# Kernel optimization log

Hardware: AMD Instinct MI355X
Metric: run time of the kernel (lower is better)

The kernel has to match this reference:

```python
import jax, jax.numpy as jnp
import numpy as np

B, FEAT = 2048, 256
NUM_PIDS, CQ_SIZE = 30000, 8192
MOMENTUM = 0.5
SCALAR = 30.0
EPS_BN = 1e-5      # BatchNorm1d default eps
EPS_NORM = 1e-12   # F.normalize default eps


def l2norm(x):
    n = jnp.linalg.norm(x, axis=1, keepdims=True)
    return x / jnp.maximum(n, EPS_NORM)


def setup_inputs() -> dict:
    key = jax.random.key(0)
    k1, k2, k3, k4 = jax.random.split(key, 4)
    inputs = jax.random.normal(k1, (B, FEAT), jnp.float32)
    label = jax.random.randint(k2, (B,), 0, NUM_PIDS + 1)  # NUM_PIDS == ignore_index
    lut = jax.random.normal(k3, (NUM_PIDS, FEAT), jnp.float32)
    cq = jax.random.normal(k4, (CQ_SIZE, FEAT), jnp.float32)
    bn_weight = jnp.ones((FEAT,), jnp.float32)
    bn_bias = jnp.zeros((FEAT,), jnp.float32)
    return {"inputs": inputs, "label": label, "lut": lut, "cq": cq,
            "bn_weight": bn_weight, "bn_bias": bn_bias}


def reference(inputs, label, lut, cq, bn_weight, bn_bias):
    dtype = inputs.dtype
    rows = jnp.arange(B)

    # --- eval-mode BN on inputs (running stats at init: mean=0, var=1) ---
    norm_inputs = inputs / jnp.sqrt(jnp.asarray(1.0 + EPS_BN, dtype)) * bn_weight + bn_bias

    # --- bad-row masks (rows that are all zero) ---
    bad_lut_mask = jnp.all(lut == 0, axis=1)            # [P]
    good_lut = ~bad_lut_mask
    lc = jnp.minimum(label, NUM_PIDS - 1)
    bad_pos_mask = (label < NUM_PIDS) & bad_lut_mask[lc]  # label hits a bad lut row

    # --- train-mode masked BN over good lut rows (momentum=1.0 => running stats = batch stats) ---
    gm = good_lut[:, None].astype(dtype)
    n = jnp.sum(gm)
    mean = jnp.sum(lut * gm, axis=0) / n
    var = jnp.sum(((lut - mean) ** 2) * gm, axis=0) / n  # biased var for normalization
    lut_bn = jnp.where(good_lut[:, None],
                       (lut - mean) / jnp.sqrt(var + EPS_BN) * bn_weight + bn_bias,
                       lut)
    # running stats update happens under the hood (detached); unbiased var
    rm1 = jax.lax.stop_gradient(mean)
    rv1 = jax.lax.stop_gradient(var * n / (n - 1.0))

    qn = l2norm(norm_inputs)                              # [B, F]
    out_lab = qn @ l2norm(lut_bn).T                       # [B, P]
    out_lab = jnp.where(bad_lut_mask[None, :], jnp.asarray(-1.0, dtype), out_lab)
    out_lab = out_lab.at[rows, lc].set(
        jnp.where(bad_pos_mask, jnp.asarray(1.0, dtype), out_lab[rows, lc]))

    # --- eval-mode masked BN on cq using the just-updated running stats ---
    bad_cq_mask = jnp.all(cq == 0, axis=1)                # [Q]
    cq_bn = jnp.where(~bad_cq_mask[:, None],
                      (cq - rm1) / jnp.sqrt(rv1 + EPS_BN) * bn_weight + bn_bias,
                      cq)
    out_unl = qn @ l2norm(cq_bn).T                        # [B, Q]
    out_unl = jnp.where(bad_cq_mask[None, :], jnp.asarray(-1.0, dtype), out_unl)

    projected = jnp.concatenate([out_lab, out_unl], axis=1) * jnp.asarray(SCALAR, dtype)

    # --- cross entropy with ignore_index = NUM_PIDS, reduction='none', then sum/B ---
    logp = jax.nn.log_softmax(projected, axis=1)
    valid = label != NUM_PIDS
    per = -logp[rows, jnp.where(valid, label, 0)]
    per = jnp.where(valid, per, jnp.asarray(0.0, dtype))
    loss = jnp.sum(per) / B

    # --- serial momentum scatter into lut + circular-buffer enqueue into cq ---
    xs = jax.lax.stop_gradient(inputs)
    lut0 = jax.lax.stop_gradient(lut)
    cq0 = jax.lax.stop_gradient(cq)

    def step(carry, xy):
        lut_c, cq_c, hdr = carry
        x, y = xy
        is_lab = y < NUM_PIDS
        yc = jnp.minimum(y, NUM_PIDS - 1)
        new_row = jnp.where(is_lab, MOMENTUM * lut_c[yc] + (1.0 - MOMENTUM) * x, lut_c[yc])
        lut_c = lut_c.at[yc].set(new_row)
        cq_row = jnp.where(is_lab, cq_c[hdr], x)
        cq_c = cq_c.at[hdr].set(cq_row)
        hdr = jnp.where(is_lab, hdr, (hdr + 1) % CQ_SIZE)
        return (lut_c, cq_c, hdr), None

    (new_lut, new_cq, _), _ = jax.lax.scan(
        step, (lut0, cq0, jnp.asarray(0, label.dtype)), (xs, label))

    return loss, new_lut, new_cq
```

## Files before the change

kernel.cpp:

```cpp
#include <hip/hip_runtime.h>
#include <math.h>

#define NUM_PIDS 30000
#define CQ_SIZE  8192
#define BATCH    2048
#define FEAT     256
#define EPS_BN   1e-5f
#define EPS_NORM 1e-12f
#define SCALARV  30.0f

#define LUT_PAD  30080
#define NCOL     38272
#define BC       128
#define LUT_TILES 235
#define CT       299
#define RT       16
#define NWG      (CT*RT)
#define NB1      240
#define ROWS1    125
#define QPLANE   (BATCH*FEAT)

#define WS_Q1    0
#define WS_CB1   (WS_Q1 + BATCH*FEAT)
#define WS_CB2   (WS_CB1 + BATCH)
#define WS_RN2   (WS_CB2 + BATCH)
#define WS_FLAGS (WS_RN2 + 2*NCOL)
#define WS_PSUM  (WS_FLAGS + LUT_PAD)
#define WS_PSQ   (WS_PSUM + NB1*FEAT)
#define WS_PCNT  (WS_PSQ + NB1*FEAT)
#define WS_A1    (WS_PCNT + 256)
#define WS_B1    (WS_A1 + FEAT)
#define WS_A2    (WS_B1 + FEAT)
#define WS_B2    (WS_A2 + FEAT)
#define WS_ZT    (WS_B2 + FEAT)
#define WS_PART  (WS_ZT + BATCH)
#define WS_LOSS8 (WS_PART + BATCH*CT)
#define WS_XH    ((WS_LOSS8 + 8 + 3) & ~3)
#define WS_XL    (WS_XH + NCOL*FEAT/2)
#define WS_QP    (WS_XL + NCOL*FEAT/2)

typedef __bf16 bf16x8 __attribute__((ext_vector_type(8)));
typedef float  f32x4  __attribute__((ext_vector_type(4)));

__device__ __forceinline__ unsigned short f2bf(float f) {
  __bf16 h = (__bf16)f; return __builtin_bit_cast(unsigned short, h);
}
__device__ __forceinline__ float bf2f(unsigned short u) {
  __bf16 h = __builtin_bit_cast(__bf16, u); return (float)h;
}
__device__ __forceinline__ void gload_lds16(const void* g, void* l) {
  __builtin_amdgcn_global_load_lds((__attribute__((address_space(1))) void*)(g),
                                   (__attribute__((address_space(3))) void*)(l), 16, 0, 0);
}

__global__ __launch_bounds__(256) void k_stats1(const float* __restrict__ lut,
                                                float* __restrict__ ws,
                                                int* __restrict__ flags) {
  const int t = threadIdx.x;
  const int rbase = blockIdx.x * ROWS1;
  __shared__ unsigned char wz[ROWS1 * 4];
  float s = 0.f, sq = 0.f;
  for (int i = 0; i < ROWS1; ++i) {
    float v = lut[(size_t)(rbase + i) * FEAT + t];
    s += v; sq += v * v;
    unsigned long long bal = __ballot(v != 0.0f);
    if ((t & 63) == 0) wz[i * 4 + (t >> 6)] = (bal != 0ull) ? 1 : 0;
  }
  __syncthreads();
  for (int i = t; i < ROWS1; i += 256) {
    int bad = !(wz[i*4] | wz[i*4+1] | wz[i*4+2] | wz[i*4+3]);
    flags[rbase + i] = bad;
  }
  ws[WS_PSUM + blockIdx.x * FEAT + t] = s;
  ws[WS_PSQ  + blockIdx.x * FEAT + t] = sq;
  if (t == 0) {
    int cnt = 0;
    for (int i = 0; i < ROWS1; ++i)
      cnt += (wz[i*4] | wz[i*4+1] | wz[i*4+2] | wz[i*4+3]) ? 1 : 0;
    ws[WS_PCNT + blockIdx.x] = (float)cnt;
  }
}

__global__ __launch_bounds__(256) void k_stats2(const float* __restrict__ bnw,
                                                const float* __restrict__ bnb,
                                                float* __restrict__ ws) {
  const int t = threadIdx.x;
  float2* rn2 = (float2*)(ws + WS_RN2);
  float s = 0.f, sq = 0.f, n = 0.f;
  for (int b = 0; b < NB1; ++b) { s += ws[WS_PSUM + b*FEAT + t]; sq += ws[WS_PSQ + b*FEAT + t]; }
  for (int b = 0; b < NB1; ++b) n += ws[WS_PCNT + b];
  float mean = s / n;
  float var = fmaxf(sq / n - mean * mean, 0.f);
  float istd_b = rsqrtf(var + EPS_BN);
  float rv1 = var * n / (n - 1.f);
  float istd_u = rsqrtf(rv1 + EPS_BN);
  float w = bnw[t], b_ = bnb[t];
  float a1 = istd_b * w, a2 = istd_u * w;
  ws[WS_A1 + t] = a1; ws[WS_B1 + t] = b_ - mean * a1;
  ws[WS_A2 + t] = a2; ws[WS_B2 + t] = b_ - mean * a2;
  if (t < (LUT_PAD - NUM_PIDS)) rn2[NUM_PIDS + t] = make_float2(0.f, -1e30f);
}

__global__ __launch_bounds__(256) void k_prep(const float* __restrict__ lut,
                                              const float* __restrict__ cq,
                                              float* __restrict__ ws,
                                              unsigned short* __restrict__ xh,
                                              unsigned short* __restrict__ xl,
                                              float* __restrict__ out_lut,
                                              float* __restrict__ out_cq) {
  const int row = blockIdx.x * 4 + (threadIdx.x >> 6);
  const int ln = threadIdx.x & 63;
  float2* rn2 = (float2*)(ws + WS_RN2);
  if (row >= NUM_PIDS && row < LUT_PAD) {
    uint2 z = make_uint2(0u, 0u);
    *(uint2*)(xh + (size_t)row * FEAT + ln * 4) = z;
    *(uint2*)(xl + (size_t)row * FEAT + ln * 4) = z;
    return;
  }
  const float* src; const float* av; const float* bv; float* dst;
  if (row < NUM_PIDS) {
    src = lut + (size_t)row * FEAT; av = ws + WS_A1; bv = ws + WS_B1;
    dst = out_lut + (size_t)row * FEAT;
  } else {
    src = cq + (size_t)(row - LUT_PAD) * FEAT; av = ws + WS_A2; bv = ws + WS_B2;
    dst = out_cq + (size_t)(row - LUT_PAD) * FEAT;
  }
  float4 x = ((const float4*)src)[ln];
  float4 a = ((const float4*)av)[ln];
  float4 b = ((const float4*)bv)[ln];
  dst[ln*4+0] = x.x; dst[ln*4+1] = x.y; dst[ln*4+2] = x.z; dst[ln*4+3] = x.w;
  unsigned short h0 = f2bf(x.x), h1 = f2bf(x.y), h2 = f2bf(x.z), h3 = f2bf(x.w);
  unsigned short l0 = f2bf(x.x - bf2f(h0)), l1 = f2bf(x.y - bf2f(h1));
  unsigned short l2 = f2bf(x.z - bf2f(h2)), l3 = f2bf(x.w - bf2f(h3));
  *(uint2*)(xh + (size_t)row * FEAT + ln * 4) =
      make_uint2((unsigned)h0 | ((unsigned)h1 << 16), (unsigned)h2 | ((unsigned)h3 << 16));
  *(uint2*)(xl + (size_t)row * FEAT + ln * 4) =
      make_uint2((unsigned)l0 | ((unsigned)l1 << 16), (unsigned)l2 | ((unsigned)l3 << 16));
  bool nz = (x.x != 0.f) || (x.y != 0.f) || (x.z != 0.f) || (x.w != 0.f);
  unsigned long long bal = __ballot(nz);
  float t0 = a.x*x.x + b.x, t1 = a.y*x.y + b.y, t2 = a.z*x.z + b.z, t3 = a.w*x.w + b.w;
  float ssum = t0*t0 + t1*t1 + t2*t2 + t3*t3;
  for (int o = 32; o; o >>= 1) ssum += __shfl_xor(ssum, o);
  if (ln == 0) {
    rn2[row] = (bal == 0ull) ? make_float2(0.f, -SCALARV)
                             : make_float2(1.0f / fmaxf(sqrtf(ssum), EPS_NORM), 1e30f);
  }
}

__global__ __launch_bounds__(256) void k_qn(const float* __restrict__ inp,
                                            const float* __restrict__ bnw,
                                            const float* __restrict__ bnb,
                                            const int* __restrict__ label,
                                            const float* __restrict__ lut,
                                            float* __restrict__ ws,
                                            unsigned short* __restrict__ qp) {
  const int r = blockIdx.x, t = threadIdx.x;
  const float s0 = rsqrtf(1.0f + EPS_BN);
  float v = inp[(size_t)r * FEAT + t];
  float bn = v * (bnw[t] * s0) + bnb[t];
  float x = bn * bn;
  for (int o = 32; o; o >>= 1) x += __shfl_down(x, o);
  __shared__ float w4[4];
  __shared__ float w8[8];
  __shared__ float w4b[4];
  if ((t & 63) == 0) w4[t >> 6] = x;
  __syncthreads();
  float nsq = w4[0] + w4[1] + w4[2] + w4[3];
  float rinv = 1.0f / fmaxf(sqrtf(nsq), EPS_NORM);
  float qn = bn * rinv;
  float y1 = qn * ws[WS_B1 + t], y2 = qn * ws[WS_B2 + t];
  for (int o = 32; o; o >>= 1) { y1 += __shfl_down(y1, o); y2 += __shfl_down(y2, o); }
  if ((t & 63) == 0) { w8[t >> 6] = y1; w8[4 + (t >> 6)] = y2; }
  float q1 = qn * ws[WS_A1 + t], q2 = qn * ws[WS_A2 + t];
  size_t o1 = (size_t)r * FEAT + t;
  unsigned short h1 = f2bf(q1), h2 = f2bf(q2);
  qp[0*QPLANE + o1] = h1;
  qp[1*QPLANE + o1] = f2bf(q1 - bf2f(h1));
  qp[2*QPLANE + o1] = h2;
  qp[3*QPLANE + o1] = f2bf(q2 - bf2f(h2));
  __syncthreads();
  if (t == 0) {
    ws[WS_CB1 + r] = w8[0] + w8[1] + w8[2] + w8[3];
    ws[WS_CB2 + r] = w8[4] + w8[5] + w8[6] + w8[7];
  }
  const int* flags = (const int*)(ws + WS_FLAGS);
  const float2* rn2 = (const float2*)(ws + WS_RN2);
  int y = label[r];
  if (y >= NUM_PIDS) { if (t == 0) ws[WS_ZT + r] = 0.f; return; }
  if (flags[y] == 1) { if (t == 0) ws[WS_ZT + r] = SCALARV; return; }
  float xt = q1 * lut[(size_t)y * FEAT + t];
  for (int o = 32; o; o >>= 1) xt += __shfl_down(xt, o);
  if ((t & 63) == 0) w4b[t >> 6] = xt;
  __syncthreads();
  if (t == 0) {
    float dot = w4b[0] + w4b[1] + w4b[2] + w4b[3];
    float cb1 = w8[0] + w8[1] + w8[2] + w8[3];
    ws[WS_ZT + r] = SCALARV * rn2[y].x * (dot + cb1);
  }
}

__global__ __launch_bounds__(256) void k_gemm(const unsigned short* __restrict__ xh,
                                              const unsigned short* __restrict__ xl,
                                              const unsigned short* __restrict__ qp,
                                              float* __restrict__ ws) {
  __shared__ __align__(16) unsigned char smem[65536];
  const int tid = threadIdx.x;
  const int w = tid >> 6, l = tid & 63;
  const int bid = blockIdx.x;
  const int sid = (bid & 7) * (NWG / 8) + (bid >> 3);
  const int colT = sid >> 4, rowT = sid & 15;
  const bool islut = colT < LUT_TILES;
  const int colbase = colT * BC;
  const int rowbase = rowT * 128;

  const unsigned short* qh = qp + (islut ? 0 : 2) * QPLANE;
  const unsigned short* ql = qh + QPLANE;

  const int segc = l >> 3, slot = l & 7;
  const int kc8l = slot ^ segc;
  const unsigned short* gsrc;
  unsigned char* lbase;
  int gbase;
  if (w == 0)      { gsrc = xh; lbase = smem;         gbase = colbase; }
  else if (w == 1) { gsrc = xl; lbase = smem + 16384; gbase = colbase; }
  else if (w == 2) { gsrc = qh; lbase = smem + 32768; gbase = rowbase; }
  else             { gsrc = ql; lbase = smem + 49152; gbase = rowbase; }

  const int lc = l & 15, lk = l >> 4;
  const int wr = w >> 1, wc = w & 1;

  f32x4 acc[4][4];
#pragma unroll
  for (int rf = 0; rf < 4; ++rf)
#pragma unroll
    for (int cf = 0; cf < 4; ++cf) { f32x4 z = {0.f,0.f,0.f,0.f}; acc[rf][cf] = z; }

  for (int kc = 0; kc < 4; ++kc) {
    const int kb = kc * 64;
#pragma unroll
    for (int i = 0; i < 16; ++i) {
      const unsigned short* g = gsrc + (size_t)(gbase + i * 8 + segc) * FEAT + kb + kc8l * 8;
      gload_lds16(g, lbase + i * 1024);
    }
    __syncthreads();
#pragma unroll
    for (int ks = 0; ks < 2; ++ks) {
      const int kc8 = ks * 4 + lk;
      const int sA = (kc8 ^ (lc & 7)) * 16;
      bf16x8 ah[4], al[4], bh[4], bl[4];
#pragma unroll
      for (int rf = 0; rf < 4; ++rf) {
        int off = (wr * 64 + rf * 16 + lc) * 128 + sA;
        ah[rf] = *(const bf16x8*)(smem + 32768 + off);
        al[rf] = *(const bf16x8*)(smem + 49152 + off);
      }
#pragma unroll
      for (int cf = 0; cf < 4; ++cf) {
        int off = (wc * 64 + cf * 16 + lc) * 128 + sA;
        bh[cf] = *(const bf16x8*)(smem + off);
        bl[cf] = *(const bf16x8*)(smem + 16384 + off);
      }
#pragma unroll
      for (int rf = 0; rf < 4; ++rf)
#pragma unroll
        for (int cf = 0; cf < 4; ++cf) {
          acc[rf][cf] = __builtin_amdgcn_mfma_f32_16x16x32_bf16(ah[rf], bh[cf], acc[rf][cf], 0, 0, 0);
          acc[rf][cf] = __builtin_amdgcn_mfma_f32_16x16x32_bf16(ah[rf], bl[cf], acc[rf][cf], 0, 0, 0);
          acc[rf][cf] = __builtin_amdgcn_mfma_f32_16x16x32_bf16(al[rf], bh[cf], acc[rf][cf], 0, 0, 0);
        }
    }
    __syncthreads();
  }

  const float* cb = ws + (islut ? WS_CB1 : WS_CB2);
  const float2* rn2 = (const float2*)(ws + WS_RN2);
  float* red = (float*)smem;
#pragma unroll
  for (int rf = 0; rf < 4; ++rf) {
    float cbv[4];
#pragma unroll
    for (int r4 = 0; r4 < 4; ++r4)
      cbv[r4] = cb[rowbase + wr * 64 + rf * 16 + lk * 4 + r4];
    float part[4] = {0.f, 0.f, 0.f, 0.f};
#pragma unroll
    for (int cf = 0; cf < 4; ++cf) {
      float2 rc = rn2[colbase + wc * 64 + cf * 16 + lc];
#pragma unroll
      for (int r4 = 0; r4 < 4; ++r4) {
        float z = SCALARV * rc.x * (acc[rf][cf][r4] + cbv[r4]);
        z = fminf(z, rc.y);
        part[r4] += __expf(z - SCALARV);
      }
    }
#pragma unroll
    for (int r4 = 0; r4 < 4; ++r4) {
#pragma unroll
      for (int o = 1; o < 16; o <<= 1) part[r4] += __shfl_xor(part[r4], o);
      if (lc == 0) red[(wr * 64 + rf * 16 + lk * 4 + r4) * 2 + wc] = part[r4];
    }
  }
  __syncthreads();
  if (tid < 128) {
    float val = red[tid * 2] + red[tid * 2 + 1];
    ws[WS_PART + (size_t)colT * BATCH + rowbase + tid] = val;
  }
}

__global__ __launch_bounds__(256) void k_loss(const int* __restrict__ label,
                                              float* __restrict__ ws) {
  const int t = threadIdx.x;
  const int r = blockIdx.x * 256 + t;
  const int* flags = (const int*)(ws + WS_FLAGS);
  float ls = 0.f;
  int y = label[r];
  if (y < NUM_PIDS) {
    float ss = 0.f;
    const float* p = ws + WS_PART;
    for (int c = 0; c < CT; ++c) ss += p[(size_t)c * BATCH + r];
    if (flags[y] == 1) ss += 1.0f - __expf(-2.0f * SCALARV);
    ls = (SCALARV + __logf(ss)) - ws[WS_ZT + r];
  }
  for (int o = 32; o; o >>= 1) ls += __shfl_down(ls, o);
  __shared__ float w4[4];
  if ((t & 63) == 0) w4[t >> 6] = ls;
  __syncthreads();
  if (t == 0) ws[WS_LOSS8 + blockIdx.x] = w4[0] + w4[1] + w4[2] + w4[3];
}

__global__ void k_loss2(float* __restrict__ ws, float* __restrict__ out) {
  if (threadIdx.x == 0) {
    float s = 0.f;
    for (int i = 0; i < 8; ++i) s += ws[WS_LOSS8 + i];
    out[0] = s / (float)BATCH;
  }
}

__global__ __launch_bounds__(256) void k_lutcq(const int* __restrict__ label,
                                               const float* __restrict__ inp,
                                               const float* __restrict__ lut,
                                               float* __restrict__ out_lut,
                                               float* __restrict__ out_cq) {
  const int r = blockIdx.x, t = threadIdx.x;
  const int y = label[r];
  __shared__ unsigned long long mask[32];
  const int wv = t >> 6, ln = t & 63;
  const int wr_ = r >> 6, br_ = r & 63;
  if (y < NUM_PIDS) {
#pragma unroll
    for (int it = 0; it < 8; ++it) {
      int i = it * 256 + wv * 64 + ln;
      unsigned long long bal = __ballot(label[i] == y);
      if (ln == 0) mask[it * 4 + wv] = bal;
    }
    __syncthreads();
    unsigned long long selfbit = 1ull << br_;
    bool after = (mask[wr_] & ~((selfbit - 1) | selfbit)) != 0ull;
    for (int w2 = wr_ + 1; w2 < 32; ++w2) after = after || (mask[w2] != 0ull);
    if (after) return;
    float f = lut[(size_t)y * FEAT + t];
    for (int w2 = 0; w2 <= wr_; ++w2) {
      unsigned long long m = mask[w2];
      if (w2 == wr_) m &= (selfbit - 1) | selfbit;
      while (m) {
        int b = __ffsll((unsigned long long)m) - 1;
        m &= m - 1;
        int rr = w2 * 64 + b;
        f = 0.5f * f + 0.5f * inp[(size_t)rr * FEAT + t];
      }
    }
    out_lut[(size_t)y * FEAT + t] = f;
  } else {
#pragma unroll
    for (int it = 0; it < 8; ++it) {
      int i = it * 256 + wv * 64 + ln;
      unsigned long long bal = __ballot(label[i] == NUM_PIDS);
      if (ln == 0) mask[it * 4 + wv] = bal;
    }
    __syncthreads();
    int rank = 0;
    for (int w2 = 0; w2 < wr_; ++w2) rank += __popcll(mask[w2]);
    rank += __popcll(mask[wr_] & ((1ull << br_) - 1ull));
    out_cq[(size_t)rank * FEAT + t] = inp[(size_t)r * FEAT + t];
  }
}

extern "C" void kernel_launch(void* const* d_in, const int* in_sizes, int n_in,
                              void* d_out, int out_size, void* d_ws, size_t ws_size,
                              hipStream_t stream) {
  const float* inp = (const float*)d_in[0];
  const int* label = (const int*)d_in[1];
  const float* lut = (const float*)d_in[2];
  const float* cq  = (const float*)d_in[3];
  const float* bnw = (const float*)d_in[4];
  const float* bnb = (const float*)d_in[5];
  float* out = (float*)d_out;
  float* ws  = (float*)d_ws;
  int* flags = (int*)(ws + WS_FLAGS);
  unsigned short* xh = (unsigned short*)(ws + WS_XH);
  unsigned short* xl = (unsigned short*)(ws + WS_XL);
  unsigned short* qp = (unsigned short*)(ws + WS_QP);

  float* out_lut = out + 1;
  float* out_cq  = out + 1 + (size_t)NUM_PIDS * FEAT;

  k_stats1<<<NB1, 256, 0, stream>>>(lut, ws, flags);
  k_stats2<<<1, 256, 0, stream>>>(bnw, bnb, ws);
  k_prep<<<NCOL / 4, 256, 0, stream>>>(lut, cq, ws, xh, xl, out_lut, out_cq);
  k_qn<<<BATCH, 256, 0, stream>>>(inp, bnw, bnb, label, lut, ws, qp);
  k_lutcq<<<BATCH, 256, 0, stream>>>(label, inp, lut, out_lut, out_cq);
  k_gemm<<<NWG, 256, 0, stream>>>(xh, xl, qp, ws);
  k_loss<<<8, 256, 0, stream>>>(label, ws);
  k_loss2<<<1, 64, 0, stream>>>(ws, out);
}
```

Before: 347.4 us.

## Switch GEMM to 32x32 MFMA tiles and parallelize LUT stats reductions

```diff
diff --git a/kernel.cpp b/kernel.cpp
--- a/kernel.cpp
+++ b/kernel.cpp
@@ -16,8 +16,8 @@
 #define CT       299
 #define RT       16
 #define NWG      (CT*RT)
-#define NB1      240
-#define ROWS1    125
+#define NB1      600
+#define ROWS1    50
 #define QPLANE   (BATCH*FEAT)
 
 #define WS_Q1    0
@@ -28,7 +28,7 @@
 #define WS_PSUM  (WS_FLAGS + LUT_PAD)
 #define WS_PSQ   (WS_PSUM + NB1*FEAT)
 #define WS_PCNT  (WS_PSQ + NB1*FEAT)
-#define WS_A1    (WS_PCNT + 256)
+#define WS_A1    (WS_PCNT + 640)
 #define WS_B1    (WS_A1 + FEAT)
 #define WS_A2    (WS_B1 + FEAT)
 #define WS_B2    (WS_A2 + FEAT)
@@ -40,7 +40,7 @@
 #define WS_QP    (WS_XL + NCOL*FEAT/2)
 
 typedef __bf16 bf16x8 __attribute__((ext_vector_type(8)));
-typedef float  f32x4  __attribute__((ext_vector_type(4)));
+typedef float  f32x16 __attribute__((ext_vector_type(16)));
 
 __device__ __forceinline__ unsigned short f2bf(float f) {
   __bf16 h = (__bf16)f; return __builtin_bit_cast(unsigned short, h);
@@ -84,21 +84,35 @@
 __global__ __launch_bounds__(256) void k_stats2(const float* __restrict__ bnw,
                                                 const float* __restrict__ bnb,
                                                 float* __restrict__ ws) {
-  const int t = threadIdx.x;
+  const int fl = threadIdx.x & 31;
+  const int p  = threadIdx.x >> 5;
+  const int f  = blockIdx.x * 32 + fl;
   float2* rn2 = (float2*)(ws + WS_RN2);
+  __shared__ float ps[8][32], pq[8][32], pn[8];
   float s = 0.f, sq = 0.f, n = 0.f;
-  for (int b = 0; b < NB1; ++b) { s += ws[WS_PSUM + b*FEAT + t]; sq += ws[WS_PSQ + b*FEAT + t]; }
-  for (int b = 0; b < NB1; ++b) n += ws[WS_PCNT + b];
-  float mean = s / n;
-  float var = fmaxf(sq / n - mean * mean, 0.f);
-  float istd_b = rsqrtf(var + EPS_BN);
-  float rv1 = var * n / (n - 1.f);
-  float istd_u = rsqrtf(rv1 + EPS_BN);
-  float w = bnw[t], b_ = bnb[t];
-  float a1 = istd_b * w, a2 = istd_u * w;
-  ws[WS_A1 + t] = a1; ws[WS_B1 + t] = b_ - mean * a1;
-  ws[WS_A2 + t] = a2; ws[WS_B2 + t] = b_ - mean * a2;
-  if (t < (LUT_PAD - NUM_PIDS)) rn2[NUM_PIDS + t] = make_float2(0.f, -1e30f);
+  for (int b = p; b < NB1; b += 8) {
+    s  += ws[WS_PSUM + b * FEAT + f];
+    sq += ws[WS_PSQ  + b * FEAT + f];
+    n  += ws[WS_PCNT + b];
+  }
+  ps[p][fl] = s; pq[p][fl] = sq;
+  if (fl == 0) pn[p] = n;
+  __syncthreads();
+  if (p == 0) {
+    float S = 0.f, SQ = 0.f, N = 0.f;
+    for (int i = 0; i < 8; ++i) { S += ps[i][fl]; SQ += pq[i][fl]; N += pn[i]; }
+    float mean = S / N;
+    float var = fmaxf(SQ / N - mean * mean, 0.f);
+    float istd_b = rsqrtf(var + EPS_BN);
+    float rv1 = var * N / (N - 1.f);
+    float istd_u = rsqrtf(rv1 + EPS_BN);
+    float w = bnw[f], b_ = bnb[f];
+    float a1 = istd_b * w, a2 = istd_u * w;
+    ws[WS_A1 + f] = a1; ws[WS_B1 + f] = b_ - mean * a1;
+    ws[WS_A2 + f] = a2; ws[WS_B2 + f] = b_ - mean * a2;
+  }
+  if (blockIdx.x == 0 && threadIdx.x < (LUT_PAD - NUM_PIDS))
+    rn2[NUM_PIDS + threadIdx.x] = make_float2(0.f, -1e30f);
 }
 
 __global__ __launch_bounds__(256) void k_prep(const float* __restrict__ lut,
@@ -226,14 +240,14 @@
   else if (w == 2) { gsrc = qh; lbase = smem + 32768; gbase = rowbase; }
   else             { gsrc = ql; lbase = smem + 49152; gbase = rowbase; }
 
-  const int lc = l & 15, lk = l >> 4;
   const int wr = w >> 1, wc = w & 1;
-
-  f32x4 acc[4][4];
-#pragma unroll
-  for (int rf = 0; rf < 4; ++rf)
-#pragma unroll
-    for (int cf = 0; cf < 4; ++cf) { f32x4 z = {0.f,0.f,0.f,0.f}; acc[rf][cf] = z; }
+  const int l31 = l & 31, lhi = l >> 5;
+
+  f32x16 acc[2][2];
+#pragma unroll
+  for (int af = 0; af < 2; ++af)
+#pragma unroll
+    for (int cf = 0; cf < 2; ++cf) acc[af][cf] = (f32x16)(0.f);
 
   for (int kc = 0; kc < 4; ++kc) {
     const int kb = kc * 64;
@@ -244,29 +258,29 @@
     }
     __syncthreads();
 #pragma unroll
-    for (int ks = 0; ks < 2; ++ks) {
-      const int kc8 = ks * 4 + lk;
-      const int sA = (kc8 ^ (lc & 7)) * 16;
-      bf16x8 ah[4], al[4], bh[4], bl[4];
-#pragma unroll
-      for (int rf = 0; rf < 4; ++rf) {
-        int off = (wr * 64 + rf * 16 + lc) * 128 + sA;
-        ah[rf] = *(const bf16x8*)(smem + 32768 + off);
-        al[rf] = *(const bf16x8*)(smem + 49152 + off);
+    for (int kt = 0; kt < 4; ++kt) {
+      const int kc8 = kt * 2 + lhi;
+      const int sA = (kc8 ^ (l & 7)) * 16;
+      bf16x8 ah[2], al[2], bh[2], bl[2];
+#pragma unroll
+      for (int af = 0; af < 2; ++af) {
+        int off = (wr * 64 + af * 32 + l31) * 128 + sA;
+        ah[af] = *(const bf16x8*)(smem + 32768 + off);
+        al[af] = *(const bf16x8*)(smem + 49152 + off);
       }
 #pragma unroll
-      for (int cf = 0; cf < 4; ++cf) {
-        int off = (wc * 64 + cf * 16 + lc) * 128 + sA;
+      for (int cf = 0; cf < 2; ++cf) {
+        int off = (wc * 64 + cf * 32 + l31) * 128 + sA;
         bh[cf] = *(const bf16x8*)(smem + off);
         bl[cf] = *(const bf16x8*)(smem + 16384 + off);
       }
 #pragma unroll
-      for (int rf = 0; rf < 4; ++rf)
-#pragma unroll
-        for (int cf = 0; cf < 4; ++cf) {
-          acc[rf][cf] = __builtin_amdgcn_mfma_f32_16x16x32_bf16(ah[rf], bh[cf], acc[rf][cf], 0, 0, 0);
-          acc[rf][cf] = __builtin_amdgcn_mfma_f32_16x16x32_bf16(ah[rf], bl[cf], acc[rf][cf], 0, 0, 0);
-          acc[rf][cf] = __builtin_amdgcn_mfma_f32_16x16x32_bf16(al[rf], bh[cf], acc[rf][cf], 0, 0, 0);
+      for (int af = 0; af < 2; ++af)
+#pragma unroll
+        for (int cf = 0; cf < 2; ++cf) {
+          acc[af][cf] = __builtin_amdgcn_mfma_f32_32x32x16_bf16(ah[af], bh[cf], acc[af][cf], 0, 0, 0);
+          acc[af][cf] = __builtin_amdgcn_mfma_f32_32x32x16_bf16(ah[af], bl[cf], acc[af][cf], 0, 0, 0);
+          acc[af][cf] = __builtin_amdgcn_mfma_f32_32x32x16_bf16(al[af], bh[cf], acc[af][cf], 0, 0, 0);
         }
     }
     __syncthreads();
@@ -275,29 +289,42 @@
   const float* cb = ws + (islut ? WS_CB1 : WS_CB2);
   const float2* rn2 = (const float2*)(ws + WS_RN2);
   float* red = (float*)smem;
-#pragma unroll
-  for (int rf = 0; rf < 4; ++rf) {
-    float cbv[4];
-#pragma unroll
-    for (int r4 = 0; r4 < 4; ++r4)
-      cbv[r4] = cb[rowbase + wr * 64 + rf * 16 + lk * 4 + r4];
-    float part[4] = {0.f, 0.f, 0.f, 0.f};
-#pragma unroll
-    for (int cf = 0; cf < 4; ++cf) {
-      float2 rc = rn2[colbase + wc * 64 + cf * 16 + lc];
-#pragma unroll
-      for (int r4 = 0; r4 < 4; ++r4) {
-        float z = SCALARV * rc.x * (acc[rf][cf][r4] + cbv[r4]);
+  const int rws = rowbase + wr * 64 + 4 * lhi;
+  float cbv[2][16], part[2][16];
+#pragma unroll
+  for (int af = 0; af < 2; ++af)
+#pragma unroll
+    for (int g = 0; g < 16; ++g) {
+      cbv[af][g] = cb[rws + af * 32 + (g & 3) + 8 * (g >> 2)];
+      part[af][g] = 0.f;
+    }
+#pragma unroll
+  for (int cf = 0; cf < 2; ++cf) {
+    float2 rc = rn2[colbase + wc * 64 + cf * 32 + l31];
+#pragma unroll
+    for (int af = 0; af < 2; ++af)
+#pragma unroll
+      for (int g = 0; g < 16; ++g) {
+        float z = SCALARV * rc.x * (acc[af][cf][g] + cbv[af][g]);
         z = fminf(z, rc.y);
-        part[r4] += __expf(z - SCALARV);
+        part[af][g] += __expf(z - SCALARV);
       }
-    }
-#pragma unroll
-    for (int r4 = 0; r4 < 4; ++r4) {
-#pragma unroll
-      for (int o = 1; o < 16; o <<= 1) part[r4] += __shfl_xor(part[r4], o);
-      if (lc == 0) red[(wr * 64 + rf * 16 + lk * 4 + r4) * 2 + wc] = part[r4];
-    }
+  }
+#pragma unroll
+  for (int o = 1; o < 32; o <<= 1)
+#pragma unroll
+    for (int af = 0; af < 2; ++af)
+#pragma unroll
+      for (int g = 0; g < 16; ++g)
+        part[af][g] += __shfl_xor(part[af][g], o);
+  if (l31 == 0) {
+#pragma unroll
+    for (int af = 0; af < 2; ++af)
+#pragma unroll
+      for (int g = 0; g < 16; ++g) {
+        int rloc = wr * 64 + af * 32 + (g & 3) + 8 * (g >> 2) + 4 * lhi;
+        red[rloc * 2 + wc] = part[af][g];
+      }
   }
   __syncthreads();
   if (tid < 128) {
@@ -404,7 +431,7 @@
   float* out_cq  = out + 1 + (size_t)NUM_PIDS * FEAT;
 
   k_stats1<<<NB1, 256, 0, stream>>>(lut, ws, flags);
-  k_stats2<<<1, 256, 0, stream>>>(bnw, bnb, ws);
+  k_stats2<<<8, 256, 0, stream>>>(bnw, bnb, ws);
   k_prep<<<NCOL / 4, 256, 0, stream>>>(lut, cq, ws, xh, xl, out_lut, out_cq);
   k_qn<<<BATCH, 256, 0, stream>>>(inp, bnw, bnb, label, lut, ws, qp);
   k_lutcq<<<BATCH, 256, 0, stream>>>(label, inp, lut, out_lut, out_cq);
```

New measurement: 331.3 us. 1.05x faster.
